# Kernel tuning notes

Hardware: AMD Instinct MI355X
Metric: run time of the kernel (lower is better)

Reference implementation:

```python
import jax, jax.numpy as jnp
import numpy as np

SCALE = 2
EPS = 1e-5  # BatchNorm2d default eps


def conv1x1(x, W, b):
    # x: [B,C,H,W], W: [O,C], b: [O]
    return jnp.einsum('bchw,oc->bohw', x, W) + b[None, :, None, None]


def maxpool(x, s):
    B, C, H, W = x.shape
    return x.reshape(B, C, H // s, s, W // s, s).max(axis=(3, 5))


def upsample_bilinear_ac(x, s):
    # bilinear upsample, align_corners=True
    B, C, H, W = x.shape
    Ho, Wo = H * s, W * s
    ys = jnp.arange(Ho) * ((H - 1) / (Ho - 1))
    xs = jnp.arange(Wo) * ((W - 1) / (Wo - 1))
    y0 = jnp.floor(ys).astype(jnp.int32)
    y1 = jnp.minimum(y0 + 1, H - 1)
    wy = (ys - y0).astype(x.dtype)
    x0 = jnp.floor(xs).astype(jnp.int32)
    x1 = jnp.minimum(x0 + 1, W - 1)
    wx = (xs - x0).astype(x.dtype)
    rows = x[:, :, y0, :] * (1 - wy)[None, None, :, None] + x[:, :, y1, :] * wy[None, None, :, None]
    return rows[:, :, :, x0] * (1 - wx) + rows[:, :, :, x1] * wx


def setup_inputs() -> dict:
    key = jax.random.key(0)
    ks = jax.random.split(key, 9)
    B, Cin, Cm, dk, H, W = 4, 64, 64, 64, 128, 128
    return {
        'x': jax.random.normal(ks[0], (B, Cin, H, W), jnp.float32),
        'memory': jax.random.normal(ks[1], (B, Cm, H, W), jnp.float32),
        'W_qkv': jax.random.normal(ks[2], (3 * dk, Cm), jnp.float32) * 0.05,
        'b_qkv': jax.random.normal(ks[3], (3 * dk,), jnp.float32) * 0.05,
        'W_out': jax.random.normal(ks[4], (Cin, dk), jnp.float32) * 0.05,
        'b_out': jax.random.normal(ks[5], (Cin,), jnp.float32) * 0.05,
        'bn_gamma': jax.random.uniform(ks[6], (Cin,), jnp.float32, 0.5, 1.5),
        'bn_beta': jax.random.normal(ks[7], (Cin,), jnp.float32) * 0.05,
        'gamma': jax.random.normal(ks[8], (1,), jnp.float32) * 0.1,
    }


def reference(x, memory, W_qkv, b_qkv, W_out, b_out, bn_gamma, bn_beta, gamma):
    d_k = W_qkv.shape[0] // 3
    qkv = conv1x1(memory, W_qkv, b_qkv)
    qkv = maxpool(qkv, SCALE)
    q, k, v = jnp.split(qkv, 3, axis=1)
    B, C, H, W = v.shape
    q = q.reshape(B, C, H * W).transpose(0, 2, 1)  # [B,N,C]
    k = k.reshape(B, C, H * W)                      # [B,C,N]
    v = v.reshape(B, C, H * W).transpose(0, 2, 1)   # [B,N,C]
    scale = jnp.asarray(d_k, x.dtype) ** 0.5
    attn = jax.nn.softmax(jnp.einsum('bnc,bcm->bnm', q, k) / scale, axis=-1)
    S = jnp.einsum('bnm,bmc->bnc', attn, v).transpose(0, 2, 1).reshape(B, C, H, W)
    S = upsample_bilinear_ac(S, SCALE)
    S = conv1x1(S, W_out, b_out)
    # BatchNorm2d (training mode: biased batch stats over B,H,W)
    mean = S.mean(axis=(0, 2, 3), keepdims=True)
    var = S.var(axis=(0, 2, 3), keepdims=True)
    S = (S - mean) / jnp.sqrt(var + EPS) * bn_gamma[None, :, None, None] + bn_beta[None, :, None, None]
    return x + gamma[0] * S
```

## Files before the change

### kernel.cpp

```cpp
#include <hip/hip_runtime.h>
#include <stdint.h>

typedef unsigned short u16;
typedef unsigned int   u32;
typedef __attribute__((ext_vector_type(8))) __bf16 bf16x8;
typedef __attribute__((ext_vector_type(4))) float  f32x4;
typedef __attribute__((ext_vector_type(2))) float  f32x2;
typedef __attribute__((ext_vector_type(4))) u32    u32x4;
typedef __attribute__((ext_vector_type(2))) u32    u32x2;

#define QSCALE 0.18033688011112042f

__device__ __forceinline__ u16 f2bf(float x) {
  u32 u = __builtin_bit_cast(u32, x);
  u = (u + 0x7FFFu + ((u >> 16) & 1u)) >> 16;
  return (u16)u;
}

__device__ __forceinline__ u32 cvt_pk_bf16(float lo, float hi) {
  u32 r;
  asm("v_cvt_pk_bf16_f32 %0, %1, %2" : "=v"(r) : "v"(lo), "v"(hi));
  return r;
}

__global__ __launch_bounds__(512) void k_qkvpool(
    const float* __restrict__ mem, const float* __restrict__ Wqkv,
    const float* __restrict__ bqkv, const float* __restrict__ Wout,
    u16* __restrict__ Q, u16* __restrict__ K, u16* __restrict__ V,
    float* __restrict__ stats)
{
  const int oy = blockIdx.x, b = blockIdx.y, t = threadIdx.x;
  const int w = t >> 6, l4 = t & 15, lh = (t >> 4) & 3;
  const int wq = w & 3, wp = w >> 2;

  if (oy == 0 && b == 0 && t < 128) stats[t] = 0.f;

  __shared__ __align__(16) u16 lds[49152];
  u16* mlds  = lds;
  u16* wlds  = lds + 16384;
  u16* qlds  = lds + 28672;
  u16* klds  = lds + 32768;
  u16* vldsT = lds + 36864;
  u16* wolds = lds + 40960;
  u16* vplds = lds + 45056;

  float bias[3][4];
  #pragma unroll
  for (int j = 0; j < 3; ++j)
    #pragma unroll
    for (int r = 0; r < 4; ++r) {
      int oc = wq * 48 + 16 * j + lh * 4 + r;
      float bv = bqkv[oc];
      bias[j][r] = (oc < 64) ? bv * QSCALE : bv;
    }

  {
    const float* src = mem + ((size_t)b * 64) * 16384 + 2 * oy * 128;
    #pragma unroll
    for (int i = 0; i < 8; ++i) {
      int g = t + 512 * i;
      int px = g & 255, c0 = (g >> 8) * 4;
      float f0 = src[(size_t)(c0 + 0) * 16384 + px];
      float f1 = src[(size_t)(c0 + 1) * 16384 + px];
      float f2 = src[(size_t)(c0 + 2) * 16384 + px];
      float f3 = src[(size_t)(c0 + 3) * 16384 + px];
      u32x2 pk;
      pk[0] = (u32)f2bf(f0) | ((u32)f2bf(f1) << 16);
      pk[1] = (u32)f2bf(f2) | ((u32)f2bf(f3) << 16);
      *(u32x2*)(mlds + px * 64 + (((c0 * 2) ^ ((px & 7) << 4)) >> 1)) = pk;
    }
  }
  {
    #pragma unroll
    for (int i = 0; i < 6; ++i) {
      int g = t + 512 * i;
      int oc = g >> 4, c0 = (g & 15) * 4;
      f32x4 wv = *(const f32x4*)(Wqkv + oc * 64 + c0);
      u32x2 pk;
      pk[0] = (u32)f2bf(wv[0]) | ((u32)f2bf(wv[1]) << 16);
      pk[1] = (u32)f2bf(wv[2]) | ((u32)f2bf(wv[3]) << 16);
      *(u32x2*)(wlds + oc * 64 + (((c0 * 2) ^ ((oc & 7) << 4)) >> 1)) = pk;
    }
  }
  {
    #pragma unroll
    for (int i = 0; i < 2; ++i) {
      int g = t + 512 * i;
      int oc = g >> 4, c0 = (g & 15) * 4;
      f32x4 wv = *(const f32x4*)(Wout + oc * 64 + c0);
      u32x2 pk;
      pk[0] = (u32)f2bf(wv[0]) | ((u32)f2bf(wv[1]) << 16);
      pk[1] = (u32)f2bf(wv[2]) | ((u32)f2bf(wv[3]) << 16);
      *(u32x2*)(wolds + oc * 64 + (((c0 * 2) ^ ((oc & 7) << 4)) >> 1)) = pk;
    }
  }
  __syncthreads();

  const int sw  = (l4 & 7) << 4;
  const int oF0 = ((lh * 16) ^ sw) >> 1;
  const int oF1 = ((64 + lh * 16) ^ sw) >> 1;
  bf16x8 af[3][2];
  #pragma unroll
  for (int j = 0; j < 3; ++j) {
    const u16* ar = wlds + (wq * 48 + 16 * j + l4) * 64;
    af[j][0] = *(const bf16x8*)(ar + oF0);
    af[j][1] = *(const bf16x8*)(ar + oF1);
  }

  #pragma unroll 2
  for (int tpi = 0; tpi < 4; ++tpi) {
    const int tp = wp * 4 + tpi;
    const u16* br0 = mlds + (16 * tp + l4) * 64;
    const u16* br1 = mlds + (128 + 16 * tp + l4) * 64;
    bf16x8 b00 = *(const bf16x8*)(br0 + oF0);
    bf16x8 b01 = *(const bf16x8*)(br0 + oF1);
    bf16x8 b10 = *(const bf16x8*)(br1 + oF0);
    bf16x8 b11 = *(const bf16x8*)(br1 + oF1);
    const int ox = 8 * tp + (l4 >> 1);
    #pragma unroll
    for (int j = 0; j < 3; ++j) {
      f32x4 a0 = {0, 0, 0, 0}, a1 = {0, 0, 0, 0};
      a0 = __builtin_amdgcn_mfma_f32_16x16x32_bf16(af[j][0], b00, a0, 0, 0, 0);
      a0 = __builtin_amdgcn_mfma_f32_16x16x32_bf16(af[j][1], b01, a0, 0, 0, 0);
      a1 = __builtin_amdgcn_mfma_f32_16x16x32_bf16(af[j][0], b10, a1, 0, 0, 0);
      a1 = __builtin_amdgcn_mfma_f32_16x16x32_bf16(af[j][1], b11, a1, 0, 0, 0);
      const int ocj = wq * 48 + 16 * j;
      const float sc = (ocj < 64) ? QSCALE : 1.0f;
      #pragma unroll
      for (int r = 0; r < 4; ++r) {
        float m = fmaxf(a0[r], a1[r]);
        m = fmaxf(m, __shfl_xor(m, 1, 64));
        u16 val = f2bf(m * sc + bias[j][r]);
        if ((l4 & 1) == 0) {
          int oc = ocj + lh * 4 + r;
          if (ocj < 64)       qlds[ox * 64 + oc]        = val;
          else if (ocj < 128) klds[ox * 64 + (oc - 64)] = val;
          else {
            int vch = oc - 128;
            vldsT[ox * 64 + (((vch * 2) ^ ((ox & 7) << 4)) >> 1)] = val;
          }
        }
      }
    }
  }
  __syncthreads();

  {
    const u16* ar = wolds + (wq * 16 + l4) * 64;
    bf16x8 aw0 = *(const bf16x8*)(ar + oF0);
    bf16x8 aw1 = *(const bf16x8*)(ar + oF1);
    #pragma unroll
    for (int nti = 0; nti < 2; ++nti) {
      const int nt = wp * 2 + nti;
      const u16* brow = vldsT + (nt * 16 + l4) * 64;
      bf16x8 bw0 = *(const bf16x8*)(brow + oF0);
      bf16x8 bw1 = *(const bf16x8*)(brow + oF1);
      f32x4 u = {0, 0, 0, 0};
      u = __builtin_amdgcn_mfma_f32_16x16x32_bf16(aw0, bw0, u, 0, 0, 0);
      u = __builtin_amdgcn_mfma_f32_16x16x32_bf16(aw1, bw1, u, 0, 0, 0);
      #pragma unroll
      for (int r = 0; r < 4; ++r) {
        int oc = wq * 16 + lh * 4 + r;
        vplds[oc * 64 + nt * 16 + l4] = f2bf(u[r]);
      }
    }
  }
  __syncthreads();

  {
    int r = t >> 3, e8 = (t & 7) * 8;
    size_t nb = (size_t)oy * 64;
    *(u32x4*)(Q + ((size_t)b * 4096 + nb + r) * 64 + e8) = *(const u32x4*)(qlds + r * 64 + e8);
    *(u32x4*)(K + ((size_t)b * 4096 + nb + r) * 64 + e8) = *(const u32x4*)(klds + r * 64 + e8);
    *(u32x4*)(V + ((size_t)b * 64 + r) * 4096 + nb + e8) = *(const u32x4*)(vplds + r * 64 + e8);
  }
}

__global__ __launch_bounds__(1024, 4) void k_attn(
    const u16* __restrict__ Q, const u16* __restrict__ K,
    const u16* __restrict__ V, const float* __restrict__ bo,
    float* __restrict__ Sa)
{
  const int qb = blockIdx.x, b = blockIdx.y, t = threadIdx.x;
  const int w = t >> 6, l4 = t & 15, lh = (t >> 4) & 3;
  const int sgrp = w >> 2, wq = w & 3;

  __shared__ __align__(16) u16 kvbuf[16384 + 18432];

  u16* kt_w = kvbuf + sgrp * 4096;
  u16* vt_w = kvbuf + 16384 + sgrp * 4608;

  const int qrow = qb * 64 + wq * 16 + l4;
  const u16* qp = Q + ((size_t)b * 4096 + qrow) * 64 + lh * 8;
  bf16x8 qa0 = *(const bf16x8*)qp;
  bf16x8 qa1 = *(const bf16x8*)(qp + 32);

  f32x4 ot[4] = {{0,0,0,0},{0,0,0,0},{0,0,0,0},{0,0,0,0}};
  float lr = 0.f;

  const int tl = t & 255;
  const int skr = tl >> 2, skc = tl & 3;
  const u16* kgp = K + ((size_t)b * 4096 + sgrp * 1024 + skr) * 64 + skc * 16;
  const u16* vgp = V + ((size_t)b * 64 + skr) * 4096 + sgrp * 1024 + skc * 16;
  const u32 fbw = (u32)(((skr & 3) | (((skr >> 3) & 1) << 2)) << 4);
  u16* kwp0 = kt_w + skr * 64 + ((((u32)(skc * 32))      ^ fbw) >> 1);
  u16* kwp1 = kt_w + skr * 64 + ((((u32)(skc * 32 + 16)) ^ fbw) >> 1);
  u16* vwp  = vt_w + skr * 72 + skc * 16;

  const int rbase = ((l4 >> 2) << 3) + (l4 & 3);
  const int fbr   = ((l4 & 3) | (((l4 >> 2) & 1) << 2)) << 4;
  const int offL  = ((lh * 16) ^ fbr) >> 1;
  const int offH  = offL ^ 32;

  u32x4 rk0 = *(const u32x4*)kgp;
  u32x4 rk1 = *(const u32x4*)(kgp + 8);
  u32x4 rv0 = *(const u32x4*)vgp;
  u32x4 rv1 = *(const u32x4*)(vgp + 8);

  #pragma unroll 1
  for (int kti = 0; kti < 16; ++kti) {
    *(u32x4*)kwp0 = rk0;
    *(u32x4*)kwp1 = rk1;
    *(u32x4*)vwp = rv0;
    *(u32x4*)(vwp + 8) = rv1;
    __syncthreads();

    if (kti < 15) {
      rk0 = *(const u32x4*)(kgp + (kti + 1) * 4096);
      rk1 = *(const u32x4*)(kgp + (kti + 1) * 4096 + 8);
      rv0 = *(const u32x4*)(vgp + (kti + 1) * 64);
      rv1 = *(const u32x4*)(vgp + (kti + 1) * 64 + 8);
    }

    #pragma unroll
    for (int ss = 0; ss < 2; ++ss) {
      const u16* kr0 = kt_w + (ss * 32 + rbase) * 64;
      const u16* kr1 = kr0 + 4 * 64;
      bf16x8 vf0 = *(const bf16x8*)(vt_w + (l4)      * 72 + ss * 32 + lh * 8);
      bf16x8 vf1 = *(const bf16x8*)(vt_w + (16 + l4) * 72 + ss * 32 + lh * 8);
      bf16x8 vf2 = *(const bf16x8*)(vt_w + (32 + l4) * 72 + ss * 32 + lh * 8);
      bf16x8 vf3 = *(const bf16x8*)(vt_w + (48 + l4) * 72 + ss * 32 + lh * 8);
      bf16x8 k00 = *(const bf16x8*)(kr0 + offL);
      bf16x8 k01 = *(const bf16x8*)(kr0 + offH);
      bf16x8 k10 = *(const bf16x8*)(kr1 + offL);
      bf16x8 k11 = *(const bf16x8*)(kr1 + offH);

      f32x4 s0 = {0, 0, 0, 0}, s1 = {0, 0, 0, 0};
      s0 = __builtin_amdgcn_mfma_f32_16x16x32_bf16(k00, qa0, s0, 0, 0, 0);
      s0 = __builtin_amdgcn_mfma_f32_16x16x32_bf16(k01, qa1, s0, 0, 0, 0);
      s1 = __builtin_amdgcn_mfma_f32_16x16x32_bf16(k10, qa0, s1, 0, 0, 0);
      s1 = __builtin_amdgcn_mfma_f32_16x16x32_bf16(k11, qa1, s1, 0, 0, 0);

      float p0[4], p1[4];
      #pragma unroll
      for (int r = 0; r < 4; ++r) {
        p0[r] = exp2f(s0[r]);
        p1[r] = exp2f(s1[r]);
        lr += p0[r] + p1[r];
      }
      u32x4 pw;
      pw[0] = cvt_pk_bf16(p0[0], p0[1]);
      pw[1] = cvt_pk_bf16(p0[2], p0[3]);
      pw[2] = cvt_pk_bf16(p1[0], p1[1]);
      pw[3] = cvt_pk_bf16(p1[2], p1[3]);
      bf16x8 pf = __builtin_bit_cast(bf16x8, pw);

      ot[0] = __builtin_amdgcn_mfma_f32_16x16x32_bf16(vf0, pf, ot[0], 0, 0, 0);
      ot[1] = __builtin_amdgcn_mfma_f32_16x16x32_bf16(vf1, pf, ot[1], 0, 0, 0);
      ot[2] = __builtin_amdgcn_mfma_f32_16x16x32_bf16(vf2, pf, ot[2], 0, 0, 0);
      ot[3] = __builtin_amdgcn_mfma_f32_16x16x32_bf16(vf3, pf, ot[3], 0, 0, 0);
    }
    __syncthreads();
  }

  lr += __shfl_xor(lr, 16, 64);
  lr += __shfl_xor(lr, 32, 64);

  float* opb = (float*)kvbuf;
  float* mlb = (float*)(kvbuf + 32768);
  #pragma unroll
  for (int d = 0; d < 4; ++d)
    #pragma unroll
    for (int r = 0; r < 4; ++r)
      opb[w * 1024 + (16 * d + lh * 4 + r) * 16 + l4] = ot[d][r];
  if (lh == 0) mlb[w * 16 + l4] = lr;
  __syncthreads();

  const int ch = t >> 4, q0v = (t & 15) * 4;
  const float bout_c = bo[ch];
  f32x4 res;
  #pragma unroll
  for (int j = 0; j < 4; ++j) {
    int q = q0v + j, wq2 = q >> 4, ql = q & 15;
    float L = mlb[(wq2)*16      + ql] + mlb[(4 + wq2)*16  + ql]
            + mlb[(8 + wq2)*16  + ql] + mlb[(12 + wq2)*16 + ql];
    float O = opb[(wq2)*1024      + ch * 16 + ql]
            + opb[(4 + wq2)*1024  + ch * 16 + ql]
            + opb[(8 + wq2)*1024  + ch * 16 + ql]
            + opb[(12 + wq2)*1024 + ch * 16 + ql];
    res[j] = O / L + bout_c;
  }
  *(f32x4*)(Sa + ((size_t)b * 64 + ch) * 4096 + (size_t)qb * 64 + q0v) = res;
}

__global__ __launch_bounds__(1024) void k_stats(const float* __restrict__ U,
                                                float* __restrict__ stats)
{
  const int c = blockIdx.x & 63, b = blockIdx.x >> 6, t = threadIdx.x;
  __shared__ __align__(16) float up[4096];
  __shared__ float red[32];
  *(f32x4*)&up[t * 4] = *(const f32x4*)(U + ((size_t)b * 64 + c) * 4096 + t * 4);
  __syncthreads();
  const float R = 0.49606299212598425f;
  float sum = 0.f, ssq = 0.f;
  #pragma unroll
  for (int i = 0; i < 4; ++i) {
    const int px0 = i * 4096 + t * 4;
    const int yo = px0 >> 7, xo0 = px0 & 127;
    float ys = yo * R; int y0 = (int)ys; float wy = ys - y0;
    int y1 = min(y0 + 1, 63);
    const float* r0 = up + y0 * 64; const float* r1 = up + y1 * 64;
    #pragma unroll
    for (int j = 0; j < 4; ++j) {
      int xo = xo0 + j;
      float xs = xo * R; int x0 = (int)xs; float wx = xs - x0;
      int x1 = min(x0 + 1, 63);
      float v0 = r0[x0] * (1.f - wx) + r0[x1] * wx;
      float v1 = r1[x0] * (1.f - wx) + r1[x1] * wx;
      float v = v0 * (1.f - wy) + v1 * wy;
      sum += v; ssq += v * v;
    }
  }
  #pragma unroll
  for (int d = 32; d >= 1; d >>= 1) {
    sum += __shfl_down(sum, d, 64);
    ssq += __shfl_down(ssq, d, 64);
  }
  if ((t & 63) == 0) { red[t >> 6] = sum; red[16 + (t >> 6)] = ssq; }
  __syncthreads();
  if (t == 0) {
    float s = 0.f, q = 0.f;
    #pragma unroll
    for (int i = 0; i < 16; ++i) { s += red[i]; q += red[16 + i]; }
    atomicAdd(&stats[c], s);
    atomicAdd(&stats[64 + c], q);
  }
}

__global__ __launch_bounds__(1024) void k_apply(
    const float* __restrict__ U, const float* __restrict__ stats,
    const float* __restrict__ x, const float* __restrict__ bng,
    const float* __restrict__ bnb, const float* __restrict__ gam,
    float* __restrict__ out)
{
  const int c = blockIdx.x & 63, b = blockIdx.x >> 6, t = threadIdx.x;
  __shared__ __align__(16) float up[4096];
  *(f32x4*)&up[t * 4] = *(const f32x4*)(U + ((size_t)b * 64 + c) * 4096 + t * 4);
  __syncthreads();
  const float inv = 1.0f / 65536.0f;
  float mean = stats[c] * inv;
  float var  = stats[64 + c] * inv - mean * mean;
  float rsig = rsqrtf(var + 1e-5f);
  float g = gam[0];
  float A  = g * bng[c] * rsig;
  float Bc = g * (bnb[c] - mean * rsig * bng[c]);
  const float R = 0.49606299212598425f;
  const size_t base = ((size_t)b * 64 + c) * 16384;
  #pragma unroll
  for (int i = 0; i < 4; ++i) {
    const int px0 = i * 4096 + t * 4;
    const int yo = px0 >> 7, xo0 = px0 & 127;
    float ys = yo * R; int y0 = (int)ys; float wy = ys - y0;
    int y1 = min(y0 + 1, 63);
    const float* r0 = up + y0 * 64; const float* r1 = up + y1 * 64;
    f32x4 xv = *(const f32x4*)(x + base + px0);
    f32x4 ov;
    #pragma unroll
    for (int j = 0; j < 4; ++j) {
      int xo = xo0 + j;
      float xs = xo * R; int x0 = (int)xs; float wx = xs - x0;
      int x1 = min(x0 + 1, 63);
      float v0 = r0[x0] * (1.f - wx) + r0[x1] * wx;
      float v1 = r1[x0] * (1.f - wx) + r1[x1] * wx;
      float v = v0 * (1.f - wy) + v1 * wy;
      ov[j] = xv[j] + v * A + Bc;
    }
    *(f32x4*)(out + base + px0) = ov;
  }
}

extern "C" void kernel_launch(void* const* d_in, const int* in_sizes, int n_in,
                              void* d_out, int out_size, void* d_ws, size_t ws_size,
                              hipStream_t stream)
{
  const float* x      = (const float*)d_in[0];
  const float* memory = (const float*)d_in[1];
  const float* Wqkv   = (const float*)d_in[2];
  const float* bqkv   = (const float*)d_in[3];
  const float* Wout   = (const float*)d_in[4];
  const float* bout   = (const float*)d_in[5];
  const float* bng    = (const float*)d_in[6];
  const float* bnb    = (const float*)d_in[7];
  const float* gamma  = (const float*)d_in[8];

  char* ws = (char*)d_ws;
  u16*   Q     = (u16*)(ws + 0);
  u16*   Kk    = (u16*)(ws + (2u << 20));
  u16*   Vt    = (u16*)(ws + (4u << 20));
  float* U     = (float*)(ws + (10u << 20));
  float* stats = (float*)(ws + (14u << 20));
  float* out   = (float*)d_out;

  k_qkvpool<<<dim3(64, 4), 512, 0, stream>>>(memory, Wqkv, bqkv, Wout, Q, Kk, Vt, stats);
  k_attn   <<<dim3(64, 4), 1024, 0, stream>>>(Q, Kk, Vt, bout, U);
  k_stats  <<<256, 1024, 0, stream>>>(U, stats);
  k_apply  <<<256, 1024, 0, stream>>>(U, stats, x, bng, bnb, gamma, out);
}
```

Measured before the change: 61.25 us.

## Pre-swizzle K/V tiles and stream them into LDS with double-buffered direct loads

The QKV producer now writes K and V in a pre-swizzled, tile-contiguous layout. The attention kernel can then copy each tile straight from global memory into LDS with global_load_lds, skipping the trip through registers. The K/V LDS buffer is double-buffered so the next tile loads while the current one is computed, and one barrier per iteration replaces two. This cuts register staging and synchronisation, at the cost of LDS growing to 128KB per block, which limits blocks per CU. It also relies on the async LDS loads being correctly waited on at the barrier.

```diff
diff --git a/kernel.cpp b/kernel.cpp
--- a/kernel.cpp
+++ b/kernel.cpp
@@ -21,6 +21,12 @@
   u32 r;
   asm("v_cvt_pk_bf16_f32 %0, %1, %2" : "=v"(r) : "v"(lo), "v"(hi));
   return r;
+}
+
+__device__ __forceinline__ void gld16(const u16* g, u16* l) {
+  __builtin_amdgcn_global_load_lds(
+      (const __attribute__((address_space(1))) void*)g,
+      (__attribute__((address_space(3))) void*)l, 16, 0, 0);
 }
 
 __global__ __launch_bounds__(512) void k_qkvpool(
@@ -171,8 +177,11 @@
     int r = t >> 3, e8 = (t & 7) * 8;
     size_t nb = (size_t)oy * 64;
     *(u32x4*)(Q + ((size_t)b * 4096 + nb + r) * 64 + e8) = *(const u32x4*)(qlds + r * 64 + e8);
-    *(u32x4*)(K + ((size_t)b * 4096 + nb + r) * 64 + e8) = *(const u32x4*)(klds + r * 64 + e8);
-    *(u32x4*)(V + ((size_t)b * 64 + r) * 4096 + nb + e8) = *(const u32x4*)(vplds + r * 64 + e8);
+    int fbK = (r & 3) | (((r >> 3) & 1) << 2);
+    int ksw = ((e8 * 2) ^ (fbK << 4)) >> 1;
+    *(u32x4*)(K + ((size_t)b * 64 + oy) * 4096 + r * 64 + ksw) = *(const u32x4*)(klds + r * 64 + e8);
+    int vsw2 = ((e8 * 2) ^ ((r & 7) << 4)) >> 1;
+    *(u32x4*)(V + ((size_t)b * 64 + oy) * 4096 + r * 64 + vsw2) = *(const u32x4*)(vplds + r * 64 + e8);
   }
 }
 
@@ -183,12 +192,24 @@
 {
   const int qb = blockIdx.x, b = blockIdx.y, t = threadIdx.x;
   const int w = t >> 6, l4 = t & 15, lh = (t >> 4) & 3;
+  const int lane = t & 63;
   const int sgrp = w >> 2, wq = w & 3;
 
-  __shared__ __align__(16) u16 kvbuf[16384 + 18432];
-
-  u16* kt_w = kvbuf + sgrp * 4096;
-  u16* vt_w = kvbuf + 16384 + sgrp * 4608;
+  __shared__ __align__(16) u16 kvbuf[65536];
+
+  const int kofs = sgrp * 4096 + wq * 1024;
+  const int vofs = 16384 + sgrp * 4096 + wq * 1024;
+  const u16* kimg = K + ((size_t)b * 64 + sgrp * 16) * 4096 + wq * 1024 + lane * 8;
+  const u16* vimg = V + ((size_t)b * 64 + sgrp * 16) * 4096 + wq * 1024 + lane * 8;
+
+#define STAGE(BUF, KTI) {                                                     \
+    const u16* kg = kimg + (size_t)(KTI) * 4096;                              \
+    const u16* vg = vimg + (size_t)(KTI) * 4096;                              \
+    gld16(kg,       (BUF) + kofs);                                            \
+    gld16(kg + 512, (BUF) + kofs + 512);                                      \
+    gld16(vg,       (BUF) + vofs);                                            \
+    gld16(vg + 512, (BUF) + vofs + 512);                                      \
+  }
 
   const int qrow = qb * 64 + wq * 16 + l4;
   const u16* qp = Q + ((size_t)b * 4096 + qrow) * 64 + lh * 8;
@@ -198,80 +219,61 @@
   f32x4 ot[4] = {{0,0,0,0},{0,0,0,0},{0,0,0,0},{0,0,0,0}};
   float lr = 0.f;
 
-  const int tl = t & 255;
-  const int skr = tl >> 2, skc = tl & 3;
-  const u16* kgp = K + ((size_t)b * 4096 + sgrp * 1024 + skr) * 64 + skc * 16;
-  const u16* vgp = V + ((size_t)b * 64 + skr) * 4096 + sgrp * 1024 + skc * 16;
-  const u32 fbw = (u32)(((skr & 3) | (((skr >> 3) & 1) << 2)) << 4);
-  u16* kwp0 = kt_w + skr * 64 + ((((u32)(skc * 32))      ^ fbw) >> 1);
-  u16* kwp1 = kt_w + skr * 64 + ((((u32)(skc * 32 + 16)) ^ fbw) >> 1);
-  u16* vwp  = vt_w + skr * 72 + skc * 16;
-
   const int rbase = ((l4 >> 2) << 3) + (l4 & 3);
   const int fbr   = ((l4 & 3) | (((l4 >> 2) & 1) << 2)) << 4;
   const int offL  = ((lh * 16) ^ fbr) >> 1;
   const int offH  = offL ^ 32;
 
-  u32x4 rk0 = *(const u32x4*)kgp;
-  u32x4 rk1 = *(const u32x4*)(kgp + 8);
-  u32x4 rv0 = *(const u32x4*)vgp;
-  u32x4 rv1 = *(const u32x4*)(vgp + 8);
+#define ATTN_COMPUTE(BB)                                                      \
+    _Pragma("unroll")                                                         \
+    for (int ss = 0; ss < 2; ++ss) {                                          \
+      const u16* kbase = (BB) + sgrp * 4096 + (ss * 32 + rbase) * 64;         \
+      const u16* vbase = (BB) + 16384 + sgrp * 4096;                          \
+      const int vswz = (((ss * 64 + lh * 16) ^ ((l4 & 7) << 4)) >> 1);        \
+      bf16x8 vf0 = *(const bf16x8*)(vbase + (l4)      * 64 + vswz);           \
+      bf16x8 vf1 = *(const bf16x8*)(vbase + (16 + l4) * 64 + vswz);           \
+      bf16x8 vf2 = *(const bf16x8*)(vbase + (32 + l4) * 64 + vswz);           \
+      bf16x8 vf3 = *(const bf16x8*)(vbase + (48 + l4) * 64 + vswz);           \
+      bf16x8 k00 = *(const bf16x8*)(kbase + offL);                            \
+      bf16x8 k01 = *(const bf16x8*)(kbase + offH);                            \
+      bf16x8 k10 = *(const bf16x8*)(kbase + 256 + offL);                      \
+      bf16x8 k11 = *(const bf16x8*)(kbase + 256 + offH);                      \
+      f32x4 s0 = {0, 0, 0, 0}, s1 = {0, 0, 0, 0};                             \
+      s0 = __builtin_amdgcn_mfma_f32_16x16x32_bf16(k00, qa0, s0, 0, 0, 0);    \
+      s0 = __builtin_amdgcn_mfma_f32_16x16x32_bf16(k01, qa1, s0, 0, 0, 0);    \
+      s1 = __builtin_amdgcn_mfma_f32_16x16x32_bf16(k10, qa0, s1, 0, 0, 0);    \
+      s1 = __builtin_amdgcn_mfma_f32_16x16x32_bf16(k11, qa1, s1, 0, 0, 0);    \
+      float p0[4], p1[4];                                                     \
+      _Pragma("unroll")                                                       \
+      for (int r = 0; r < 4; ++r) {                                           \
+        p0[r] = exp2f(s0[r]);                                                 \
+        p1[r] = exp2f(s1[r]);                                                 \
+        lr += p0[r] + p1[r];                                                  \
+      }                                                                       \
+      u32x4 pw;                                                               \
+      pw[0] = cvt_pk_bf16(p0[0], p0[1]);                                      \
+      pw[1] = cvt_pk_bf16(p0[2], p0[3]);                                      \
+      pw[2] = cvt_pk_bf16(p1[0], p1[1]);                                      \
+      pw[3] = cvt_pk_bf16(p1[2], p1[3]);                                      \
+      bf16x8 pf = __builtin_bit_cast(bf16x8, pw);                             \
+      ot[0] = __builtin_amdgcn_mfma_f32_16x16x32_bf16(vf0, pf, ot[0], 0, 0, 0);\
+      ot[1] = __builtin_amdgcn_mfma_f32_16x16x32_bf16(vf1, pf, ot[1], 0, 0, 0);\
+      ot[2] = __builtin_amdgcn_mfma_f32_16x16x32_bf16(vf2, pf, ot[2], 0, 0, 0);\
+      ot[3] = __builtin_amdgcn_mfma_f32_16x16x32_bf16(vf3, pf, ot[3], 0, 0, 0);\
+    }
+
+  STAGE(kvbuf, 0)
 
   #pragma unroll 1
   for (int kti = 0; kti < 16; ++kti) {
-    *(u32x4*)kwp0 = rk0;
-    *(u32x4*)kwp1 = rk1;
-    *(u32x4*)vwp = rv0;
-    *(u32x4*)(vwp + 8) = rv1;
+    u16* bufc = kvbuf + (kti & 1) * 32768;
     __syncthreads();
-
-    if (kti < 15) {
-      rk0 = *(const u32x4*)(kgp + (kti + 1) * 4096);
-      rk1 = *(const u32x4*)(kgp + (kti + 1) * 4096 + 8);
-      rv0 = *(const u32x4*)(vgp + (kti + 1) * 64);
-      rv1 = *(const u32x4*)(vgp + (kti + 1) * 64 + 8);
-    }
-
-    #pragma unroll
-    for (int ss = 0; ss < 2; ++ss) {
-      const u16* kr0 = kt_w + (ss * 32 + rbase) * 64;
-      const u16* kr1 = kr0 + 4 * 64;
-      bf16x8 vf0 = *(const bf16x8*)(vt_w + (l4)      * 72 + ss * 32 + lh * 8);
-      bf16x8 vf1 = *(const bf16x8*)(vt_w + (16 + l4) * 72 + ss * 32 + lh * 8);
-      bf16x8 vf2 = *(const bf16x8*)(vt_w + (32 + l4) * 72 + ss * 32 + lh * 8);
-      bf16x8 vf3 = *(const bf16x8*)(vt_w + (48 + l4) * 72 + ss * 32 + lh * 8);
-      bf16x8 k00 = *(const bf16x8*)(kr0 + offL);
-      bf16x8 k01 = *(const bf16x8*)(kr0 + offH);
-      bf16x8 k10 = *(const bf16x8*)(kr1 + offL);
-      bf16x8 k11 = *(const bf16x8*)(kr1 + offH);
-
-      f32x4 s0 = {0, 0, 0, 0}, s1 = {0, 0, 0, 0};
-      s0 = __builtin_amdgcn_mfma_f32_16x16x32_bf16(k00, qa0, s0, 0, 0, 0);
-      s0 = __builtin_amdgcn_mfma_f32_16x16x32_bf16(k01, qa1, s0, 0, 0, 0);
-      s1 = __builtin_amdgcn_mfma_f32_16x16x32_bf16(k10, qa0, s1, 0, 0, 0);
-      s1 = __builtin_amdgcn_mfma_f32_16x16x32_bf16(k11, qa1, s1, 0, 0, 0);
-
-      float p0[4], p1[4];
-      #pragma unroll
-      for (int r = 0; r < 4; ++r) {
-        p0[r] = exp2f(s0[r]);
-        p1[r] = exp2f(s1[r]);
-        lr += p0[r] + p1[r];
-      }
-      u32x4 pw;
-      pw[0] = cvt_pk_bf16(p0[0], p0[1]);
-      pw[1] = cvt_pk_bf16(p0[2], p0[3]);
-      pw[2] = cvt_pk_bf16(p1[0], p1[1]);
-      pw[3] = cvt_pk_bf16(p1[2], p1[3]);
-      bf16x8 pf = __builtin_bit_cast(bf16x8, pw);
-
-      ot[0] = __builtin_amdgcn_mfma_f32_16x16x32_bf16(vf0, pf, ot[0], 0, 0, 0);
-      ot[1] = __builtin_amdgcn_mfma_f32_16x16x32_bf16(vf1, pf, ot[1], 0, 0, 0);
-      ot[2] = __builtin_amdgcn_mfma_f32_16x16x32_bf16(vf2, pf, ot[2], 0, 0, 0);
-      ot[3] = __builtin_amdgcn_mfma_f32_16x16x32_bf16(vf3, pf, ot[3], 0, 0, 0);
-    }
-    __syncthreads();
-  }
+    if (kti < 15) STAGE(kvbuf + ((kti + 1) & 1) * 32768, kti + 1)
+    ATTN_COMPUTE(bufc)
+  }
+  __syncthreads();
+#undef ATTN_COMPUTE
+#undef STAGE
 
   lr += __shfl_xor(lr, 16, 64);
   lr += __shfl_xor(lr, 32, 64);
```

Result: no change. 61.17 us (-0.1%).

## Load K/V MFMA fragments directly from global memory, dropping LDS staging

Applied to the files above, without the earlier changes.

The attention kernel no longer stages K and V tiles through shared memory with a register-prefetch double buffer and two barriers per tile. Each wave now reads its K and V MFMA operand fragments straight from global memory, relying on L1/L2 caching because the four query waves in a group read the same data. This removes the LDS write/read traffic and the __syncthreads stalls, but it adds redundant global loads and exposes their latency, which is only partly hidden by unroll 2.

```diff
diff --git a/kernel.cpp b/kernel.cpp
--- a/kernel.cpp
+++ b/kernel.cpp
@@ -185,104 +185,71 @@
   const int w = t >> 6, l4 = t & 15, lh = (t >> 4) & 3;
   const int sgrp = w >> 2, wq = w & 3;
 
-  __shared__ __align__(16) u16 kvbuf[16384 + 18432];
-
-  u16* kt_w = kvbuf + sgrp * 4096;
-  u16* vt_w = kvbuf + 16384 + sgrp * 4608;
+  __shared__ __align__(16) u16 mrg[33280];
 
   const int qrow = qb * 64 + wq * 16 + l4;
   const u16* qp = Q + ((size_t)b * 4096 + qrow) * 64 + lh * 8;
   bf16x8 qa0 = *(const bf16x8*)qp;
   bf16x8 qa1 = *(const bf16x8*)(qp + 32);
 
-  f32x4 ot[4] = {{0,0,0,0},{0,0,0,0},{0,0,0,0},{0,0,0,0}};
+  f32x4 ot0 = {0,0,0,0}, ot1 = {0,0,0,0}, ot2 = {0,0,0,0}, ot3 = {0,0,0,0};
   float lr = 0.f;
 
-  const int tl = t & 255;
-  const int skr = tl >> 2, skc = tl & 3;
-  const u16* kgp = K + ((size_t)b * 4096 + sgrp * 1024 + skr) * 64 + skc * 16;
-  const u16* vgp = V + ((size_t)b * 64 + skr) * 4096 + sgrp * 1024 + skc * 16;
-  const u32 fbw = (u32)(((skr & 3) | (((skr >> 3) & 1) << 2)) << 4);
-  u16* kwp0 = kt_w + skr * 64 + ((((u32)(skc * 32))      ^ fbw) >> 1);
-  u16* kwp1 = kt_w + skr * 64 + ((((u32)(skc * 32 + 16)) ^ fbw) >> 1);
-  u16* vwp  = vt_w + skr * 72 + skc * 16;
-
   const int rbase = ((l4 >> 2) << 3) + (l4 & 3);
-  const int fbr   = ((l4 & 3) | (((l4 >> 2) & 1) << 2)) << 4;
-  const int offL  = ((lh * 16) ^ fbr) >> 1;
-  const int offH  = offL ^ 32;
-
-  u32x4 rk0 = *(const u32x4*)kgp;
-  u32x4 rk1 = *(const u32x4*)(kgp + 8);
-  u32x4 rv0 = *(const u32x4*)vgp;
-  u32x4 rv1 = *(const u32x4*)(vgp + 8);
-
-  #pragma unroll 1
-  for (int kti = 0; kti < 16; ++kti) {
-    *(u32x4*)kwp0 = rk0;
-    *(u32x4*)kwp1 = rk1;
-    *(u32x4*)vwp = rv0;
-    *(u32x4*)(vwp + 8) = rv1;
-    __syncthreads();
-
-    if (kti < 15) {
-      rk0 = *(const u32x4*)(kgp + (kti + 1) * 4096);
-      rk1 = *(const u32x4*)(kgp + (kti + 1) * 4096 + 8);
-      rv0 = *(const u32x4*)(vgp + (kti + 1) * 64);
-      rv1 = *(const u32x4*)(vgp + (kti + 1) * 64 + 8);
-    }
-
-    #pragma unroll
-    for (int ss = 0; ss < 2; ++ss) {
-      const u16* kr0 = kt_w + (ss * 32 + rbase) * 64;
-      const u16* kr1 = kr0 + 4 * 64;
-      bf16x8 vf0 = *(const bf16x8*)(vt_w + (l4)      * 72 + ss * 32 + lh * 8);
-      bf16x8 vf1 = *(const bf16x8*)(vt_w + (16 + l4) * 72 + ss * 32 + lh * 8);
-      bf16x8 vf2 = *(const bf16x8*)(vt_w + (32 + l4) * 72 + ss * 32 + lh * 8);
-      bf16x8 vf3 = *(const bf16x8*)(vt_w + (48 + l4) * 72 + ss * 32 + lh * 8);
-      bf16x8 k00 = *(const bf16x8*)(kr0 + offL);
-      bf16x8 k01 = *(const bf16x8*)(kr0 + offH);
-      bf16x8 k10 = *(const bf16x8*)(kr1 + offL);
-      bf16x8 k11 = *(const bf16x8*)(kr1 + offH);
-
-      f32x4 s0 = {0, 0, 0, 0}, s1 = {0, 0, 0, 0};
-      s0 = __builtin_amdgcn_mfma_f32_16x16x32_bf16(k00, qa0, s0, 0, 0, 0);
-      s0 = __builtin_amdgcn_mfma_f32_16x16x32_bf16(k01, qa1, s0, 0, 0, 0);
-      s1 = __builtin_amdgcn_mfma_f32_16x16x32_bf16(k10, qa0, s1, 0, 0, 0);
-      s1 = __builtin_amdgcn_mfma_f32_16x16x32_bf16(k11, qa1, s1, 0, 0, 0);
-
-      float p0[4], p1[4];
-      #pragma unroll
-      for (int r = 0; r < 4; ++r) {
-        p0[r] = exp2f(s0[r]);
-        p1[r] = exp2f(s1[r]);
-        lr += p0[r] + p1[r];
-      }
-      u32x4 pw;
-      pw[0] = cvt_pk_bf16(p0[0], p0[1]);
-      pw[1] = cvt_pk_bf16(p0[2], p0[3]);
-      pw[2] = cvt_pk_bf16(p1[0], p1[1]);
-      pw[3] = cvt_pk_bf16(p1[2], p1[3]);
-      bf16x8 pf = __builtin_bit_cast(bf16x8, pw);
-
-      ot[0] = __builtin_amdgcn_mfma_f32_16x16x32_bf16(vf0, pf, ot[0], 0, 0, 0);
-      ot[1] = __builtin_amdgcn_mfma_f32_16x16x32_bf16(vf1, pf, ot[1], 0, 0, 0);
-      ot[2] = __builtin_amdgcn_mfma_f32_16x16x32_bf16(vf2, pf, ot[2], 0, 0, 0);
-      ot[3] = __builtin_amdgcn_mfma_f32_16x16x32_bf16(vf3, pf, ot[3], 0, 0, 0);
-    }
-    __syncthreads();
+  const u16* kbg = K + ((size_t)b * 4096 + sgrp * 1024 + rbase) * 64 + lh * 8;
+  const u16* vbg = V + ((size_t)(b * 64 + l4)) * 4096 + sgrp * 1024 + lh * 8;
+
+  #pragma unroll 2
+  for (int ks = 0; ks < 32; ++ks) {
+    const u16* kp = kbg + (size_t)ks * 32 * 64;
+    bf16x8 k00 = *(const bf16x8*)(kp);
+    bf16x8 k01 = *(const bf16x8*)(kp + 32);
+    bf16x8 k10 = *(const bf16x8*)(kp + 256);
+    bf16x8 k11 = *(const bf16x8*)(kp + 256 + 32);
+    const u16* vp = vbg + ks * 32;
+    bf16x8 vf0 = *(const bf16x8*)(vp);
+    bf16x8 vf1 = *(const bf16x8*)(vp + 16 * 4096);
+    bf16x8 vf2 = *(const bf16x8*)(vp + 32 * 4096);
+    bf16x8 vf3 = *(const bf16x8*)(vp + 48 * 4096);
+
+    f32x4 s0 = {0, 0, 0, 0}, s1 = {0, 0, 0, 0};
+    s0 = __builtin_amdgcn_mfma_f32_16x16x32_bf16(k00, qa0, s0, 0, 0, 0);
+    s0 = __builtin_amdgcn_mfma_f32_16x16x32_bf16(k01, qa1, s0, 0, 0, 0);
+    s1 = __builtin_amdgcn_mfma_f32_16x16x32_bf16(k10, qa0, s1, 0, 0, 0);
+    s1 = __builtin_amdgcn_mfma_f32_16x16x32_bf16(k11, qa1, s1, 0, 0, 0);
+
+    float p0[4], p1[4];
+    #pragma unroll
+    for (int r = 0; r < 4; ++r) {
+      p0[r] = exp2f(s0[r]);
+      p1[r] = exp2f(s1[r]);
+      lr += p0[r] + p1[r];
+    }
+    u32x4 pw;
+    pw[0] = cvt_pk_bf16(p0[0], p0[1]);
+    pw[1] = cvt_pk_bf16(p0[2], p0[3]);
+    pw[2] = cvt_pk_bf16(p1[0], p1[1]);
+    pw[3] = cvt_pk_bf16(p1[2], p1[3]);
+    bf16x8 pf = __builtin_bit_cast(bf16x8, pw);
+
+    ot0 = __builtin_amdgcn_mfma_f32_16x16x32_bf16(vf0, pf, ot0, 0, 0, 0);
+    ot1 = __builtin_amdgcn_mfma_f32_16x16x32_bf16(vf1, pf, ot1, 0, 0, 0);
+    ot2 = __builtin_amdgcn_mfma_f32_16x16x32_bf16(vf2, pf, ot2, 0, 0, 0);
+    ot3 = __builtin_amdgcn_mfma_f32_16x16x32_bf16(vf3, pf, ot3, 0, 0, 0);
   }
 
   lr += __shfl_xor(lr, 16, 64);
   lr += __shfl_xor(lr, 32, 64);
 
-  float* opb = (float*)kvbuf;
-  float* mlb = (float*)(kvbuf + 32768);
-  #pragma unroll
-  for (int d = 0; d < 4; ++d)
+  float* opb = (float*)mrg;
+  float* mlb = (float*)(mrg + 32768);
+  #pragma unroll
+  for (int d = 0; d < 4; ++d) {
+    f32x4 ov = d == 0 ? ot0 : (d == 1 ? ot1 : (d == 2 ? ot2 : ot3));
     #pragma unroll
     for (int r = 0; r < 4; ++r)
-      opb[w * 1024 + (16 * d + lh * 4 + r) * 16 + l4] = ot[d][r];
+      opb[w * 1024 + (16 * d + lh * 4 + r) * 16 + l4] = ov[r];
+  }
   if (lh == 0) mlb[w * 16 + l4] = lr;
   __syncthreads();
 
```

Result: slower. 146.8 us (+139.7%).
